# Kernel tuning notes

Measured on AMD Instinct MI355X. Metric: run time of the kernel, lower is better.

## Reference

```python
import jax, jax.numpy as jnp
import numpy as np

TEMPERATURE = 12.5   # args.temperature (DeepEMD default)
EPS = 0.05           # entropic regularization for the OT (EMD) solve
N_ITERS = 100        # Sinkhorn iterations
COS_EPS = 1e-8       # F.cosine_similarity eps


def setup_inputs() -> dict:
    key = jax.random.key(0)
    k1, k2 = jax.random.split(key)
    B, C, H, W = 512, 1024, 8, 8
    proto = jax.random.normal(k1, (B, C, H, W), dtype=jnp.float32)
    query = jax.random.normal(k2, (B, C, H, W), dtype=jnp.float32)
    return {"proto": proto, "query": query}


def get_weight_vector(A, Bmap):
    """A,[b,c,h,w]; pooled Bmap reweights A's channels -> node weights [b, h*w]."""
    pooled = Bmap.mean(axis=(2, 3), keepdims=True)          # adaptive_avg_pool2d -> [b,c,1,1]
    comb = (A * pooled).sum(axis=1).reshape(A.shape[0], -1)  # [b, h*w]
    return jax.nn.relu(comb) + 0.001


def center(x):
    # args.norm == 'center': subtract channel mean
    return x - x.mean(axis=1, keepdims=True)


def cosine_sim_map(proto, query):
    """sim[b, q_node, p_node] = cosine similarity between flattened spatial nodes."""
    B, C = proto.shape[0], proto.shape[1]
    p = proto.reshape(B, C, -1).transpose(0, 2, 1)   # [b, Np, c]
    q = query.reshape(B, C, -1).transpose(0, 2, 1)   # [b, Nq, c]
    pn = p / jnp.maximum(jnp.linalg.norm(p, axis=-1, keepdims=True), COS_EPS)
    qn = q / jnp.maximum(jnp.linalg.norm(q, axis=-1, keepdims=True), COS_EPS)
    return jnp.einsum('bqc,bpc->bqp', qn, pn)        # [b, Nq, Np]


def sinkhorn_flow(cost, r, c):
    """Entropic-regularized OT flow with marginals r [b,N], c [b,M]; cost [b,N,M]."""
    K = jnp.exp(-cost / EPS)
    v0 = jnp.ones_like(c)

    def body(v, _):
        u = r / jnp.maximum(jnp.einsum('bnm,bm->bn', K, v), 1e-30)
        v = c / jnp.maximum(jnp.einsum('bnm,bn->bm', K, u), 1e-30)
        return v, None

    v, _ = jax.lax.scan(body, v0, None, length=N_ITERS)
    u = r / jnp.maximum(jnp.einsum('bnm,bm->bn', K, v), 1e-30)
    return u[:, :, None] * K * v[:, None, :]         # [b, N, M]


def reference(proto, query):
    # emd_forward(proto, query)
    weight_1 = get_weight_vector(query, proto)       # [b, Nq]
    weight_2 = get_weight_vector(proto, query)       # [b, Np]
    p = center(proto)
    q = center(query)
    sim = cosine_sim_map(p, q)                       # [b, Nq, Np]
    # get_emd_distance: solve OT on cost = 1 - sim with (normalized) node weights
    r = weight_1 / weight_1.sum(axis=-1, keepdims=True)
    c = weight_2 / weight_2.sum(axis=-1, keepdims=True)
    flow = sinkhorn_flow(1.0 - sim, r, c)
    num_node = weight_1.shape[-1]
    logits = (sim * flow).sum(axis=(-1, -2)) * (TEMPERATURE / num_node)
    return logits
```

## Files before the change

### kernel.cpp

```cpp
#include <hip/hip_runtime.h>
#include <math.h>

#define NCH    1024
#define NN     64
#define CK     32
#define NCHUNK (NCH / CK)
#define KSC    28.853900817779268f

#define STAT_Q(v) { sqp[0]+=(v).x; q2p[0]=fmaf((v).x,(v).x,q2p[0]); \
                    sqp[1]+=(v).y; q2p[1]=fmaf((v).y,(v).y,q2p[1]); \
                    sqp[2]+=(v).z; q2p[2]=fmaf((v).z,(v).z,q2p[2]); \
                    sqp[3]+=(v).w; q2p[3]=fmaf((v).w,(v).w,q2p[3]); }
#define STAT_P(v) { spp[0]+=(v).x; p2p[0]=fmaf((v).x,(v).x,p2p[0]); \
                    spp[1]+=(v).y; p2p[1]=fmaf((v).y,(v).y,p2p[1]); \
                    spp[2]+=(v).z; p2p[2]=fmaf((v).z,(v).z,p2p[2]); \
                    spp[3]+=(v).w; p2p[3]=fmaf((v).w,(v).w,p2p[3]); }

__global__ __launch_bounds__(256)
void deepemd_fused(const float* __restrict__ proto,
                   const float* __restrict__ query,
                   float* __restrict__ out)
{
    __shared__ __align__(16) float stage[2 * CK * NN];
    __shared__ __align__(16) float Kl [NN][68];
    __shared__ __align__(16) float KTl[NN][68];
    __shared__ __align__(16) float statL[4][NN];
    __shared__ __align__(16) float uL[NN];
    __shared__ __align__(16) float vL[NN];
    __shared__ __align__(16) float rL[NN];
    __shared__ __align__(16) float cL[NN];
    __shared__ float redl[4];

    const int b  = blockIdx.x;
    const int t  = threadIdx.x;
    const int tr = t >> 4;
    const int tc = t & 15;
    const int n0 = tr * 4;
    const int m0 = tc * 4;
    const int ofs = 4 * t;

    const float* __restrict__ pb = proto + (size_t)b * (NCH * NN);
    const float* __restrict__ qb = query + (size_t)b * (NCH * NN);

    float acc[4][4];
    #pragma unroll
    for (int i = 0; i < 4; ++i) {
        #pragma unroll
        for (int j = 0; j < 4; ++j) acc[i][j] = 0.0f;
    }
    float sqp[4] = {0,0,0,0}, q2p[4] = {0,0,0,0};
    float spp[4] = {0,0,0,0}, p2p[4] = {0,0,0,0};

    float4 qv0 = *(const float4*)(qb + ofs);
    float4 qv1 = *(const float4*)(qb + 1024 + ofs);
    float4 pv0 = *(const float4*)(pb + ofs);
    float4 pv1 = *(const float4*)(pb + 1024 + ofs);

    for (int ch = 0; ch < NCHUNK; ++ch) {
        if (ch) __syncthreads();
        *(float4*)&stage[       ofs] = qv0;
        *(float4*)&stage[1024 + ofs] = qv1;
        *(float4*)&stage[2048 + ofs] = pv0;
        *(float4*)&stage[3072 + ofs] = pv1;

        float4 nq0, nq1, np0, np1;
        const bool more = (ch + 1 < NCHUNK);
        if (more) {
            const float* qn = qb + (ch + 1) * 2048;
            const float* pn = pb + (ch + 1) * 2048;
            nq0 = *(const float4*)(qn + ofs);
            nq1 = *(const float4*)(qn + 1024 + ofs);
            np0 = *(const float4*)(pn + ofs);
            np1 = *(const float4*)(pn + 1024 + ofs);
        }

        STAT_Q(qv0); STAT_Q(qv1);
        STAT_P(pv0); STAT_P(pv1);

        __syncthreads();

        #pragma unroll 8
        for (int cc = 0; cc < CK; ++cc) {
            float4 a  = *(const float4*)&stage[cc * 64 + n0];
            float4 bb = *(const float4*)&stage[2048 + cc * 64 + m0];
            acc[0][0]=fmaf(a.x,bb.x,acc[0][0]); acc[0][1]=fmaf(a.x,bb.y,acc[0][1]);
            acc[0][2]=fmaf(a.x,bb.z,acc[0][2]); acc[0][3]=fmaf(a.x,bb.w,acc[0][3]);
            acc[1][0]=fmaf(a.y,bb.x,acc[1][0]); acc[1][1]=fmaf(a.y,bb.y,acc[1][1]);
            acc[1][2]=fmaf(a.y,bb.z,acc[1][2]); acc[1][3]=fmaf(a.y,bb.w,acc[1][3]);
            acc[2][0]=fmaf(a.z,bb.x,acc[2][0]); acc[2][1]=fmaf(a.z,bb.y,acc[2][1]);
            acc[2][2]=fmaf(a.z,bb.z,acc[2][2]); acc[2][3]=fmaf(a.z,bb.w,acc[2][3]);
            acc[3][0]=fmaf(a.w,bb.x,acc[3][0]); acc[3][1]=fmaf(a.w,bb.y,acc[3][1]);
            acc[3][2]=fmaf(a.w,bb.z,acc[3][2]); acc[3][3]=fmaf(a.w,bb.w,acc[3][3]);
        }
        if (more) { qv0 = nq0; qv1 = nq1; pv0 = np0; pv1 = np1; }
    }
    __syncthreads();

    #pragma unroll
    for (int i = 0; i < 4; ++i) {
        float s = acc[i][0] + acc[i][1] + acc[i][2] + acc[i][3];
        s += __shfl_xor(s, 1, 64); s += __shfl_xor(s, 2, 64);
        s += __shfl_xor(s, 4, 64); s += __shfl_xor(s, 8, 64);
        if (tc == 0) uL[n0 + i] = s;
    }
    #pragma unroll
    for (int k = 0; k < 4; ++k) {
        stage[t*16 +      k] = sqp[k];
        stage[t*16 +  4 + k] = q2p[k];
        stage[t*16 +  8 + k] = spp[k];
        stage[t*16 + 12 + k] = p2p[k];
    }
    __syncthreads();

    if (t < NN) {
        const int g = t >> 2, k = t & 3;
        float ssq = 0, sq2 = 0, ssp = 0, sp2 = 0;
        #pragma unroll
        for (int j = 0; j < 16; ++j) {
            const float* row = &stage[(j * 16 + g) * 16];
            ssq += row[k]; sq2 += row[4 + k]; ssp += row[8 + k]; sp2 += row[12 + k];
        }
        statL[0][t] = ssq; statL[1][t] = sq2; statL[2][t] = ssp; statL[3][t] = sp2;
    }
    __syncthreads();

    #pragma unroll
    for (int j = 0; j < 4; ++j) {
        float s = acc[0][j] + acc[1][j] + acc[2][j] + acc[3][j];
        stage[tr * 64 + m0 + j] = s;
    }
    __syncthreads();

    if (t < NN) {
        float cs = 0;
        #pragma unroll
        for (int i = 0; i < 16; ++i) cs += stage[i * 64 + t];
        float w2 = fmaxf(cs * (1.0f/64.0f), 0.0f) + 0.001f;
        float w1 = fmaxf(uL[t] * (1.0f/64.0f), 0.0f) + 0.001f;
        float s1 = w1, s2 = w2;
        #pragma unroll
        for (int m = 1; m < 64; m <<= 1) {
            s1 += __shfl_xor(s1, m, 64);
            s2 += __shfl_xor(s2, m, 64);
        }
        rL[t] = w1 / s1;
        cL[t] = w2 / s2;
        vL[t] = 1.0f;
    }
    __syncthreads();

    float nq_[4], np_[4], sqn[4], spm[4];
    #pragma unroll
    for (int i = 0; i < 4; ++i) {
        float sv = statL[0][n0 + i];
        float var = statL[1][n0 + i] - sv * sv * (1.0f/1024.0f);
        nq_[i] = fmaxf(sqrtf(fmaxf(var, 0.0f)), 1e-8f);
        sqn[i] = sv;
    }
    #pragma unroll
    for (int j = 0; j < 4; ++j) {
        float sv = statL[2][m0 + j];
        float var = statL[3][m0 + j] - sv * sv * (1.0f/1024.0f);
        np_[j] = fmaxf(sqrtf(fmaxf(var, 0.0f)), 1e-8f);
        spm[j] = sv;
    }
    #pragma unroll
    for (int i = 0; i < 4; ++i) {
        #pragma unroll
        for (int j = 0; j < 4; ++j) {
            float sim = (acc[i][j] - sqn[i] * spm[j] * (1.0f/1024.0f)) / (nq_[i] * np_[j]);
            acc[i][j] = sim;
            float Kv = exp2f((sim - 1.0f) * KSC);
            Kl [n0 + i][m0 + j] = Kv;
            KTl[m0 + j][n0 + i] = Kv;
        }
    }
    __syncthreads();

    const int sn  = t >> 2;
    const int sp4 = t & 3;
    float Kr[16], KTr[16];
    #pragma unroll
    for (int jj = 0; jj < 4; ++jj) {
        float4 kv = *(const float4*)&Kl [sn][sp4 * 16 + jj * 4];
        float4 kt = *(const float4*)&KTl[sn][sp4 * 16 + jj * 4];
        Kr [jj*4+0]=kv.x; Kr [jj*4+1]=kv.y; Kr [jj*4+2]=kv.z; Kr [jj*4+3]=kv.w;
        KTr[jj*4+0]=kt.x; KTr[jj*4+1]=kt.y; KTr[jj*4+2]=kt.z; KTr[jj*4+3]=kt.w;
    }
    const float rreg = rL[sn];
    const float creg = cL[sn];

    #define DOT16(KK, ARR) ({ \
        float4 x0 = *(const float4*)&ARR[sp4*16 +  0]; \
        float4 x1 = *(const float4*)&ARR[sp4*16 +  4]; \
        float4 x2 = *(const float4*)&ARR[sp4*16 +  8]; \
        float4 x3 = *(const float4*)&ARR[sp4*16 + 12]; \
        float a0 = 0.0f, a1 = 0.0f; \
        a0=fmaf(KK[0],x0.x,a0);  a1=fmaf(KK[1],x0.y,a1); \
        a0=fmaf(KK[2],x0.z,a0);  a1=fmaf(KK[3],x0.w,a1); \
        a0=fmaf(KK[4],x1.x,a0);  a1=fmaf(KK[5],x1.y,a1); \
        a0=fmaf(KK[6],x1.z,a0);  a1=fmaf(KK[7],x1.w,a1); \
        a0=fmaf(KK[8],x2.x,a0);  a1=fmaf(KK[9],x2.y,a1); \
        a0=fmaf(KK[10],x2.z,a0); a1=fmaf(KK[11],x2.w,a1); \
        a0=fmaf(KK[12],x3.x,a0); a1=fmaf(KK[13],x3.y,a1); \
        a0=fmaf(KK[14],x3.z,a0); a1=fmaf(KK[15],x3.w,a1); \
        a0 + a1; })

    for (int it = 0; it < 100; ++it) {
        float s = DOT16(Kr, vL);
        s += __shfl_xor(s, 1, 64); s += __shfl_xor(s, 2, 64);
        float u = rreg / fmaxf(s, 1e-30f);
        if (sp4 == 0) uL[sn] = u;
        __syncthreads();
        float s2 = DOT16(KTr, uL);
        s2 += __shfl_xor(s2, 1, 64); s2 += __shfl_xor(s2, 2, 64);
        float vv = creg / fmaxf(s2, 1e-30f);
        if (sp4 == 0) vL[sn] = vv;
        __syncthreads();
    }
    {
        float s = DOT16(Kr, vL);
        s += __shfl_xor(s, 1, 64); s += __shfl_xor(s, 2, 64);
        float u = rreg / fmaxf(s, 1e-30f);
        if (sp4 == 0) uL[sn] = u;
    }
    __syncthreads();

    float uu[4], vv_[4];
    #pragma unroll
    for (int i = 0; i < 4; ++i) uu[i]  = uL[n0 + i];
    #pragma unroll
    for (int j = 0; j < 4; ++j) vv_[j] = vL[m0 + j];
    float part = 0.0f;
    #pragma unroll
    for (int i = 0; i < 4; ++i) {
        #pragma unroll
        for (int j = 0; j < 4; ++j) {
            float sim = acc[i][j];
            float Kv  = exp2f((sim - 1.0f) * KSC);
            part = fmaf(sim * Kv, uu[i] * vv_[j], part);
        }
    }
    #pragma unroll
    for (int m = 1; m < 64; m <<= 1) part += __shfl_xor(part, m, 64);
    if ((t & 63) == 0) redl[t >> 6] = part;
    __syncthreads();
    if (t == 0) out[b] = (redl[0] + redl[1] + redl[2] + redl[3]) * (12.5f / 64.0f);
}

extern "C" void kernel_launch(void* const* d_in, const int* in_sizes, int n_in,
                              void* d_out, int out_size, void* d_ws, size_t ws_size,
                              hipStream_t stream) {
    const float* proto = (const float*)d_in[0];
    const float* query = (const float*)d_in[1];
    float* out = (float*)d_out;
    (void)in_sizes; (void)n_in; (void)d_ws; (void)ws_size; (void)out_size;
    deepemd_fused<<<dim3(512), dim3(256), 0, stream>>>(proto, query, out);
}
```

Measured before the change: 133.6 us.

## Split channel reduction across four blocks per batch with workspace and separate solve kernel

The single fused kernel is split into two. The first computes partial Gram matrices and channel statistics over a quarter of the channels in each of 4x as many blocks, writing them to workspace. The second sums the partials and runs the Sinkhorn solve. This raises parallelism in the bandwidth-bound reduction phase, since 512 blocks underfill the GPU, at the cost of a second launch and an extra workspace round trip of about 35 MB. If the workspace is too small, it falls back to the fused kernel.

```diff
diff --git a/kernel.cpp b/kernel.cpp
--- a/kernel.cpp
+++ b/kernel.cpp
@@ -4,8 +4,9 @@
 #define NCH    1024
 #define NN     64
 #define CK     32
-#define NCHUNK (NCH / CK)
 #define KSC    28.853900817779268f
+#define SPLIT  4
+#define WSB    4352
 
 #define STAT_Q(v) { sqp[0]+=(v).x; q2p[0]=fmaf((v).x,(v).x,q2p[0]); \
                     sqp[1]+=(v).y; q2p[1]=fmaf((v).y,(v).y,q2p[1]); \
@@ -15,6 +16,277 @@
                     spp[1]+=(v).y; p2p[1]=fmaf((v).y,(v).y,p2p[1]); \
                     spp[2]+=(v).z; p2p[2]=fmaf((v).z,(v).z,p2p[2]); \
                     spp[3]+=(v).w; p2p[3]=fmaf((v).w,(v).w,p2p[3]); }
+
+#define GRAM_CHUNK_BODY(NCHUNK_, QB_, PB_)                                     \
+    for (int ch = 0; ch < (NCHUNK_); ++ch) {                                   \
+        if (ch) __syncthreads();                                               \
+        *(float4*)&stage[       ofs] = qv0;                                    \
+        *(float4*)&stage[1024 + ofs] = qv1;                                    \
+        *(float4*)&stage[2048 + ofs] = pv0;                                    \
+        *(float4*)&stage[3072 + ofs] = pv1;                                    \
+        float4 nq0, nq1, np0, np1;                                             \
+        const bool more = (ch + 1 < (NCHUNK_));                                \
+        if (more) {                                                            \
+            const float* qn = (QB_) + (ch + 1) * 2048;                         \
+            const float* pn = (PB_) + (ch + 1) * 2048;                         \
+            nq0 = *(const float4*)(qn + ofs);                                  \
+            nq1 = *(const float4*)(qn + 1024 + ofs);                           \
+            np0 = *(const float4*)(pn + ofs);                                  \
+            np1 = *(const float4*)(pn + 1024 + ofs);                           \
+        }                                                                      \
+        STAT_Q(qv0); STAT_Q(qv1);                                              \
+        STAT_P(pv0); STAT_P(pv1);                                              \
+        __syncthreads();                                                       \
+        _Pragma("unroll 8")                                                    \
+        for (int cc = 0; cc < CK; ++cc) {                                      \
+            float4 a  = *(const float4*)&stage[cc * 64 + n0];                  \
+            float4 bb = *(const float4*)&stage[2048 + cc * 64 + m0];           \
+            acc[0][0]=fmaf(a.x,bb.x,acc[0][0]); acc[0][1]=fmaf(a.x,bb.y,acc[0][1]); \
+            acc[0][2]=fmaf(a.x,bb.z,acc[0][2]); acc[0][3]=fmaf(a.x,bb.w,acc[0][3]); \
+            acc[1][0]=fmaf(a.y,bb.x,acc[1][0]); acc[1][1]=fmaf(a.y,bb.y,acc[1][1]); \
+            acc[1][2]=fmaf(a.y,bb.z,acc[1][2]); acc[1][3]=fmaf(a.y,bb.w,acc[1][3]); \
+            acc[2][0]=fmaf(a.z,bb.x,acc[2][0]); acc[2][1]=fmaf(a.z,bb.y,acc[2][1]); \
+            acc[2][2]=fmaf(a.z,bb.z,acc[2][2]); acc[2][3]=fmaf(a.z,bb.w,acc[2][3]); \
+            acc[3][0]=fmaf(a.w,bb.x,acc[3][0]); acc[3][1]=fmaf(a.w,bb.y,acc[3][1]); \
+            acc[3][2]=fmaf(a.w,bb.z,acc[3][2]); acc[3][3]=fmaf(a.w,bb.w,acc[3][3]); \
+        }                                                                      \
+        if (more) { qv0 = nq0; qv1 = nq1; pv0 = np0; pv1 = np1; }              \
+    }
+
+#define DOT16(KK, ARR) ({ \
+    float4 x0 = *(const float4*)&ARR[sp4*16 +  0]; \
+    float4 x1 = *(const float4*)&ARR[sp4*16 +  4]; \
+    float4 x2 = *(const float4*)&ARR[sp4*16 +  8]; \
+    float4 x3 = *(const float4*)&ARR[sp4*16 + 12]; \
+    float a0 = 0.0f, a1 = 0.0f; \
+    a0=fmaf(KK[0],x0.x,a0);  a1=fmaf(KK[1],x0.y,a1); \
+    a0=fmaf(KK[2],x0.z,a0);  a1=fmaf(KK[3],x0.w,a1); \
+    a0=fmaf(KK[4],x1.x,a0);  a1=fmaf(KK[5],x1.y,a1); \
+    a0=fmaf(KK[6],x1.z,a0);  a1=fmaf(KK[7],x1.w,a1); \
+    a0=fmaf(KK[8],x2.x,a0);  a1=fmaf(KK[9],x2.y,a1); \
+    a0=fmaf(KK[10],x2.z,a0); a1=fmaf(KK[11],x2.w,a1); \
+    a0=fmaf(KK[12],x3.x,a0); a1=fmaf(KK[13],x3.y,a1); \
+    a0=fmaf(KK[14],x3.z,a0); a1=fmaf(KK[15],x3.w,a1); \
+    a0 + a1; })
+
+__global__ __launch_bounds__(256)
+void gram_partial(const float* __restrict__ proto,
+                  const float* __restrict__ query,
+                  float* __restrict__ ws)
+{
+    __shared__ __align__(16) float stage[4096];
+
+    const int bid = blockIdx.x;
+    const int b = bid >> 2, s = bid & (SPLIT - 1);
+    const int t  = threadIdx.x;
+    const int tr = t >> 4, tc = t & 15;
+    const int n0 = tr * 4, m0 = tc * 4;
+    const int ofs = 4 * t;
+
+    const float* __restrict__ pb = proto + (size_t)b * (NCH * NN) + s * (NCH / SPLIT) * NN;
+    const float* __restrict__ qb = query + (size_t)b * (NCH * NN) + s * (NCH / SPLIT) * NN;
+
+    float acc[4][4];
+    #pragma unroll
+    for (int i = 0; i < 4; ++i)
+        #pragma unroll
+        for (int j = 0; j < 4; ++j) acc[i][j] = 0.0f;
+    float sqp[4] = {0,0,0,0}, q2p[4] = {0,0,0,0};
+    float spp[4] = {0,0,0,0}, p2p[4] = {0,0,0,0};
+
+    float4 qv0 = *(const float4*)(qb + ofs);
+    float4 qv1 = *(const float4*)(qb + 1024 + ofs);
+    float4 pv0 = *(const float4*)(pb + ofs);
+    float4 pv1 = *(const float4*)(pb + 1024 + ofs);
+
+    GRAM_CHUNK_BODY(NCH / SPLIT / CK, qb, pb)
+    __syncthreads();
+
+    float* __restrict__ wsb = ws + (size_t)bid * WSB;
+    #pragma unroll
+    for (int i = 0; i < 4; ++i) {
+        float4 v; v.x = acc[i][0]; v.y = acc[i][1]; v.z = acc[i][2]; v.w = acc[i][3];
+        *(float4*)&wsb[(n0 + i) * 64 + m0] = v;
+    }
+
+    #pragma unroll
+    for (int k = 0; k < 4; ++k) {
+        stage[t*16 +      k] = sqp[k];
+        stage[t*16 +  4 + k] = q2p[k];
+        stage[t*16 +  8 + k] = spp[k];
+        stage[t*16 + 12 + k] = p2p[k];
+    }
+    __syncthreads();
+    if (t < NN) {
+        const int g = t >> 2, k = t & 3;
+        float ssq = 0, sq2 = 0, ssp = 0, sp2 = 0;
+        #pragma unroll
+        for (int j = 0; j < 16; ++j) {
+            const float* row = &stage[(j * 16 + g) * 16];
+            ssq += row[k]; sq2 += row[4 + k]; ssp += row[8 + k]; sp2 += row[12 + k];
+        }
+        wsb[4096 +   0 + t] = ssq;
+        wsb[4096 +  64 + t] = sq2;
+        wsb[4096 + 128 + t] = ssp;
+        wsb[4096 + 192 + t] = sp2;
+    }
+}
+
+__global__ __launch_bounds__(256)
+void emd_solve(const float* __restrict__ ws, float* __restrict__ out)
+{
+    __shared__ __align__(16) float stage[16 * 64];
+    __shared__ __align__(16) float Kl [NN][68];
+    __shared__ __align__(16) float KTl[NN][68];
+    __shared__ __align__(16) float statL[4][NN];
+    __shared__ __align__(16) float uL[NN];
+    __shared__ __align__(16) float vL[NN];
+    __shared__ __align__(16) float rL[NN];
+    __shared__ __align__(16) float cL[NN];
+    __shared__ float redl[4];
+
+    const int b  = blockIdx.x;
+    const int t  = threadIdx.x;
+    const int tr = t >> 4, tc = t & 15;
+    const int n0 = tr * 4, m0 = tc * 4;
+
+    const float* __restrict__ wsb = ws + (size_t)b * SPLIT * WSB;
+
+    float acc[4][4];
+    #pragma unroll
+    for (int i = 0; i < 4; ++i)
+        #pragma unroll
+        for (int j = 0; j < 4; ++j) acc[i][j] = 0.0f;
+    #pragma unroll
+    for (int s = 0; s < SPLIT; ++s) {
+        const float* __restrict__ g = wsb + s * WSB;
+        #pragma unroll
+        for (int i = 0; i < 4; ++i) {
+            float4 v = *(const float4*)&g[(n0 + i) * 64 + m0];
+            acc[i][0] += v.x; acc[i][1] += v.y; acc[i][2] += v.z; acc[i][3] += v.w;
+        }
+    }
+    if (t < NN) {
+        float s0 = 0, s1 = 0, s2 = 0, s3 = 0;
+        #pragma unroll
+        for (int s = 0; s < SPLIT; ++s) {
+            const float* __restrict__ g = wsb + s * WSB + 4096;
+            s0 += g[t]; s1 += g[64 + t]; s2 += g[128 + t]; s3 += g[192 + t];
+        }
+        statL[0][t] = s0; statL[1][t] = s1; statL[2][t] = s2; statL[3][t] = s3;
+    }
+    #pragma unroll
+    for (int i = 0; i < 4; ++i) {
+        float s = acc[i][0] + acc[i][1] + acc[i][2] + acc[i][3];
+        s += __shfl_xor(s, 1, 64); s += __shfl_xor(s, 2, 64);
+        s += __shfl_xor(s, 4, 64); s += __shfl_xor(s, 8, 64);
+        if (tc == 0) uL[n0 + i] = s;
+    }
+    #pragma unroll
+    for (int j = 0; j < 4; ++j)
+        stage[tr * 64 + m0 + j] = acc[0][j] + acc[1][j] + acc[2][j] + acc[3][j];
+    __syncthreads();
+
+    if (t < NN) {
+        float cs = 0;
+        #pragma unroll
+        for (int i = 0; i < 16; ++i) cs += stage[i * 64 + t];
+        float w2 = fmaxf(cs * (1.0f/64.0f), 0.0f) + 0.001f;
+        float w1 = fmaxf(uL[t] * (1.0f/64.0f), 0.0f) + 0.001f;
+        float s1 = w1, s2 = w2;
+        #pragma unroll
+        for (int m = 1; m < 64; m <<= 1) {
+            s1 += __shfl_xor(s1, m, 64);
+            s2 += __shfl_xor(s2, m, 64);
+        }
+        rL[t] = w1 / s1;
+        cL[t] = w2 / s2;
+        vL[t] = 1.0f;
+    }
+    {
+        float nq_[4], np_[4], sqn[4], spm[4];
+        #pragma unroll
+        for (int i = 0; i < 4; ++i) {
+            float sv  = statL[0][n0 + i];
+            float var = statL[1][n0 + i] - sv * sv * (1.0f/1024.0f);
+            nq_[i] = fmaxf(sqrtf(fmaxf(var, 0.0f)), 1e-8f);
+            sqn[i] = sv;
+        }
+        #pragma unroll
+        for (int j = 0; j < 4; ++j) {
+            float sv  = statL[2][m0 + j];
+            float var = statL[3][m0 + j] - sv * sv * (1.0f/1024.0f);
+            np_[j] = fmaxf(sqrtf(fmaxf(var, 0.0f)), 1e-8f);
+            spm[j] = sv;
+        }
+        #pragma unroll
+        for (int i = 0; i < 4; ++i) {
+            #pragma unroll
+            for (int j = 0; j < 4; ++j) {
+                float sim = (acc[i][j] - sqn[i] * spm[j] * (1.0f/1024.0f)) / (nq_[i] * np_[j]);
+                acc[i][j] = sim;
+                float Kv = exp2f((sim - 1.0f) * KSC);
+                Kl [n0 + i][m0 + j] = Kv;
+                KTl[m0 + j][n0 + i] = Kv;
+            }
+        }
+    }
+    __syncthreads();
+
+    const int sn  = t >> 2;
+    const int sp4 = t & 3;
+    float Kr[16], KTr[16];
+    #pragma unroll
+    for (int jj = 0; jj < 4; ++jj) {
+        float4 kv = *(const float4*)&Kl [sn][sp4 * 16 + jj * 4];
+        float4 kt = *(const float4*)&KTl[sn][sp4 * 16 + jj * 4];
+        Kr [jj*4+0]=kv.x; Kr [jj*4+1]=kv.y; Kr [jj*4+2]=kv.z; Kr [jj*4+3]=kv.w;
+        KTr[jj*4+0]=kt.x; KTr[jj*4+1]=kt.y; KTr[jj*4+2]=kt.z; KTr[jj*4+3]=kt.w;
+    }
+    const float rreg = rL[sn];
+    const float creg = cL[sn];
+
+    for (int it = 0; it < 100; ++it) {
+        float s = DOT16(Kr, vL);
+        s += __shfl_xor(s, 1, 64); s += __shfl_xor(s, 2, 64);
+        float u = rreg / fmaxf(s, 1e-30f);
+        if (sp4 == 0) uL[sn] = u;
+        __syncthreads();
+        float s2 = DOT16(KTr, uL);
+        s2 += __shfl_xor(s2, 1, 64); s2 += __shfl_xor(s2, 2, 64);
+        float vv = creg / fmaxf(s2, 1e-30f);
+        if (sp4 == 0) vL[sn] = vv;
+        __syncthreads();
+    }
+    {
+        float s = DOT16(Kr, vL);
+        s += __shfl_xor(s, 1, 64); s += __shfl_xor(s, 2, 64);
+        float u = rreg / fmaxf(s, 1e-30f);
+        if (sp4 == 0) uL[sn] = u;
+    }
+    __syncthreads();
+
+    float uu[4], vv_[4];
+    #pragma unroll
+    for (int i = 0; i < 4; ++i) uu[i]  = uL[n0 + i];
+    #pragma unroll
+    for (int j = 0; j < 4; ++j) vv_[j] = vL[m0 + j];
+    float part = 0.0f;
+    #pragma unroll
+    for (int i = 0; i < 4; ++i) {
+        #pragma unroll
+        for (int j = 0; j < 4; ++j) {
+            float sim = acc[i][j];
+            float Kv  = exp2f((sim - 1.0f) * KSC);
+            part = fmaf(sim * Kv, uu[i] * vv_[j], part);
+        }
+    }
+    #pragma unroll
+    for (int m = 1; m < 64; m <<= 1) part += __shfl_xor(part, m, 64);
+    if ((t & 63) == 0) redl[t >> 6] = part;
+    __syncthreads();
+    if (t == 0) out[b] = (redl[0] + redl[1] + redl[2] + redl[3]) * (12.5f / 64.0f);
+}
 
 __global__ __launch_bounds__(256)
 void deepemd_fused(const float* __restrict__ proto,
@@ -33,10 +305,8 @@
 
     const int b  = blockIdx.x;
     const int t  = threadIdx.x;
-    const int tr = t >> 4;
-    const int tc = t & 15;
-    const int n0 = tr * 4;
-    const int m0 = tc * 4;
+    const int tr = t >> 4, tc = t & 15;
+    const int n0 = tr * 4, m0 = tc * 4;
     const int ofs = 4 * t;
 
     const float* __restrict__ pb = proto + (size_t)b * (NCH * NN);
@@ -44,10 +314,9 @@
 
     float acc[4][4];
     #pragma unroll
-    for (int i = 0; i < 4; ++i) {
+    for (int i = 0; i < 4; ++i)
         #pragma unroll
         for (int j = 0; j < 4; ++j) acc[i][j] = 0.0f;
-    }
     float sqp[4] = {0,0,0,0}, q2p[4] = {0,0,0,0};
     float spp[4] = {0,0,0,0}, p2p[4] = {0,0,0,0};
 
@@ -56,44 +325,7 @@
     float4 pv0 = *(const float4*)(pb + ofs);
     float4 pv1 = *(const float4*)(pb + 1024 + ofs);
 
-    for (int ch = 0; ch < NCHUNK; ++ch) {
-        if (ch) __syncthreads();
-        *(float4*)&stage[       ofs] = qv0;
-        *(float4*)&stage[1024 + ofs] = qv1;
-        *(float4*)&stage[2048 + ofs] = pv0;
-        *(float4*)&stage[3072 + ofs] = pv1;
-
-        float4 nq0, nq1, np0, np1;
-        const bool more = (ch + 1 < NCHUNK);
-        if (more) {
-            const float* qn = qb + (ch + 1) * 2048;
-            const float* pn = pb + (ch + 1) * 2048;
-            nq0 = *(const float4*)(qn + ofs);
-            nq1 = *(const float4*)(qn + 1024 + ofs);
-            np0 = *(const float4*)(pn + ofs);
-            np1 = *(const float4*)(pn + 1024 + ofs);
-        }
-
-        STAT_Q(qv0); STAT_Q(qv1);
-        STAT_P(pv0); STAT_P(pv1);
-
-        __syncthreads();
-
-        #pragma unroll 8
-        for (int cc = 0; cc < CK; ++cc) {
-            float4 a  = *(const float4*)&stage[cc * 64 + n0];
-            float4 bb = *(const float4*)&stage[2048 + cc * 64 + m0];
-            acc[0][0]=fmaf(a.x,bb.x,acc[0][0]); acc[0][1]=fmaf(a.x,bb.y,acc[0][1]);
-            acc[0][2]=fmaf(a.x,bb.z,acc[0][2]); acc[0][3]=fmaf(a.x,bb.w,acc[0][3]);
-            acc[1][0]=fmaf(a.y,bb.x,acc[1][0]); acc[1][1]=fmaf(a.y,bb.y,acc[1][1]);
-            acc[1][2]=fmaf(a.y,bb.z,acc[1][2]); acc[1][3]=fmaf(a.y,bb.w,acc[1][3]);
-            acc[2][0]=fmaf(a.z,bb.x,acc[2][0]); acc[2][1]=fmaf(a.z,bb.y,acc[2][1]);
-            acc[2][2]=fmaf(a.z,bb.z,acc[2][2]); acc[2][3]=fmaf(a.z,bb.w,acc[2][3]);
-            acc[3][0]=fmaf(a.w,bb.x,acc[3][0]); acc[3][1]=fmaf(a.w,bb.y,acc[3][1]);
-            acc[3][2]=fmaf(a.w,bb.z,acc[3][2]); acc[3][3]=fmaf(a.w,bb.w,acc[3][3]);
-        }
-        if (more) { qv0 = nq0; qv1 = nq1; pv0 = np0; pv1 = np1; }
-    }
+    GRAM_CHUNK_BODY(NCH / CK, qb, pb)
     __syncthreads();
 
     #pragma unroll
@@ -111,7 +343,6 @@
         stage[t*16 + 12 + k] = p2p[k];
     }
     __syncthreads();
-
     if (t < NN) {
         const int g = t >> 2, k = t & 3;
         float ssq = 0, sq2 = 0, ssp = 0, sp2 = 0;
@@ -123,14 +354,10 @@
         statL[0][t] = ssq; statL[1][t] = sq2; statL[2][t] = ssp; statL[3][t] = sp2;
     }
     __syncthreads();
-
-    #pragma unroll
-    for (int j = 0; j < 4; ++j) {
-        float s = acc[0][j] + acc[1][j] + acc[2][j] + acc[3][j];
-        stage[tr * 64 + m0 + j] = s;
-    }
-    __syncthreads();
-
+    #pragma unroll
+    for (int j = 0; j < 4; ++j)
+        stage[tr * 64 + m0 + j] = acc[0][j] + acc[1][j] + acc[2][j] + acc[3][j];
+    __syncthreads();
     if (t < NN) {
         float cs = 0;
         #pragma unroll
@@ -149,30 +376,32 @@
     }
     __syncthreads();
 
-    float nq_[4], np_[4], sqn[4], spm[4];
-    #pragma unroll
-    for (int i = 0; i < 4; ++i) {
-        float sv = statL[0][n0 + i];
-        float var = statL[1][n0 + i] - sv * sv * (1.0f/1024.0f);
-        nq_[i] = fmaxf(sqrtf(fmaxf(var, 0.0f)), 1e-8f);
-        sqn[i] = sv;
-    }
-    #pragma unroll
-    for (int j = 0; j < 4; ++j) {
-        float sv = statL[2][m0 + j];
-        float var = statL[3][m0 + j] - sv * sv * (1.0f/1024.0f);
-        np_[j] = fmaxf(sqrtf(fmaxf(var, 0.0f)), 1e-8f);
-        spm[j] = sv;
-    }
-    #pragma unroll
-    for (int i = 0; i < 4; ++i) {
+    {
+        float nq_[4], np_[4], sqn[4], spm[4];
+        #pragma unroll
+        for (int i = 0; i < 4; ++i) {
+            float sv  = statL[0][n0 + i];
+            float var = statL[1][n0 + i] - sv * sv * (1.0f/1024.0f);
+            nq_[i] = fmaxf(sqrtf(fmaxf(var, 0.0f)), 1e-8f);
+            sqn[i] = sv;
+        }
         #pragma unroll
         for (int j = 0; j < 4; ++j) {
-            float sim = (acc[i][j] - sqn[i] * spm[j] * (1.0f/1024.0f)) / (nq_[i] * np_[j]);
-            acc[i][j] = sim;
-            float Kv = exp2f((sim - 1.0f) * KSC);
-            Kl [n0 + i][m0 + j] = Kv;
-            KTl[m0 + j][n0 + i] = Kv;
+            float sv  = statL[2][m0 + j];
+            float var = statL[3][m0 + j] - sv * sv * (1.0f/1024.0f);
+            np_[j] = fmaxf(sqrtf(fmaxf(var, 0.0f)), 1e-8f);
+            spm[j] = sv;
+        }
+        #pragma unroll
+        for (int i = 0; i < 4; ++i) {
+            #pragma unroll
+            for (int j = 0; j < 4; ++j) {
+                float sim = (acc[i][j] - sqn[i] * spm[j] * (1.0f/1024.0f)) / (nq_[i] * np_[j]);
+                acc[i][j] = sim;
+                float Kv = exp2f((sim - 1.0f) * KSC);
+                Kl [n0 + i][m0 + j] = Kv;
+                KTl[m0 + j][n0 + i] = Kv;
+            }
         }
     }
     __syncthreads();
@@ -189,22 +418,6 @@
     }
     const float rreg = rL[sn];
     const float creg = cL[sn];
-
-    #define DOT16(KK, ARR) ({ \
-        float4 x0 = *(const float4*)&ARR[sp4*16 +  0]; \
-        float4 x1 = *(const float4*)&ARR[sp4*16 +  4]; \
-        float4 x2 = *(const float4*)&ARR[sp4*16 +  8]; \
-        float4 x3 = *(const float4*)&ARR[sp4*16 + 12]; \
-        float a0 = 0.0f, a1 = 0.0f; \
-        a0=fmaf(KK[0],x0.x,a0);  a1=fmaf(KK[1],x0.y,a1); \
-        a0=fmaf(KK[2],x0.z,a0);  a1=fmaf(KK[3],x0.w,a1); \
-        a0=fmaf(KK[4],x1.x,a0);  a1=fmaf(KK[5],x1.y,a1); \
-        a0=fmaf(KK[6],x1.z,a0);  a1=fmaf(KK[7],x1.w,a1); \
-        a0=fmaf(KK[8],x2.x,a0);  a1=fmaf(KK[9],x2.y,a1); \
-        a0=fmaf(KK[10],x2.z,a0); a1=fmaf(KK[11],x2.w,a1); \
-        a0=fmaf(KK[12],x3.x,a0); a1=fmaf(KK[13],x3.y,a1); \
-        a0=fmaf(KK[14],x3.z,a0); a1=fmaf(KK[15],x3.w,a1); \
-        a0 + a1; })
 
     for (int it = 0; it < 100; ++it) {
         float s = DOT16(Kr, vL);
@@ -254,6 +467,13 @@
     const float* proto = (const float*)d_in[0];
     const float* query = (const float*)d_in[1];
     float* out = (float*)d_out;
-    (void)in_sizes; (void)n_in; (void)d_ws; (void)ws_size; (void)out_size;
-    deepemd_fused<<<dim3(512), dim3(256), 0, stream>>>(proto, query, out);
+    (void)in_sizes; (void)n_in; (void)out_size;
+
+    const size_t need = (size_t)512 * SPLIT * WSB * sizeof(float);
+    if (ws_size >= need) {
+        gram_partial<<<dim3(512 * SPLIT), dim3(256), 0, stream>>>(proto, query, (float*)d_ws);
+        emd_solve  <<<dim3(512),         dim3(256), 0, stream>>>((const float*)d_ws, out);
+    } else {
+        deepemd_fused<<<dim3(512), dim3(256), 0, stream>>>(proto, query, out);
+    }
 }
```

After: 134.5 us. No clear change (+0.7%).

## Split channel reduction across eight waves with 8x8 register tiles and LDS reduction

Applied to the files above, without the earlier changes.

The block grows to 512 threads, and each of the eight waves takes a separate eighth of the channels. Each wave computes a full 64x64 partial Gram tile in 8x8 per-thread register blocks, loading straight from global memory instead of going through shared-memory staging with barriers. The eight partials are then summed in LDS in a few serialized passes. This aims to remove the per-chunk barrier loop and add more memory parallelism, at the cost of more registers, a cross-wave reduction and duplicated Sinkhorn work in the upper 256 threads.

```diff
diff --git a/kernel.cpp b/kernel.cpp
--- a/kernel.cpp
+++ b/kernel.cpp
@@ -1,210 +1,213 @@
 #include <hip/hip_runtime.h>
 #include <math.h>
 
-#define NCH    1024
-#define NN     64
-#define CK     32
-#define NCHUNK (NCH / CK)
-#define KSC    28.853900817779268f
-
-#define STAT_Q(v) { sqp[0]+=(v).x; q2p[0]=fmaf((v).x,(v).x,q2p[0]); \
-                    sqp[1]+=(v).y; q2p[1]=fmaf((v).y,(v).y,q2p[1]); \
-                    sqp[2]+=(v).z; q2p[2]=fmaf((v).z,(v).z,q2p[2]); \
-                    sqp[3]+=(v).w; q2p[3]=fmaf((v).w,(v).w,q2p[3]); }
-#define STAT_P(v) { spp[0]+=(v).x; p2p[0]=fmaf((v).x,(v).x,p2p[0]); \
-                    spp[1]+=(v).y; p2p[1]=fmaf((v).y,(v).y,p2p[1]); \
-                    spp[2]+=(v).z; p2p[2]=fmaf((v).z,(v).z,p2p[2]); \
-                    spp[3]+=(v).w; p2p[3]=fmaf((v).w,(v).w,p2p[3]); }
-
-__global__ __launch_bounds__(256)
-void deepemd_fused(const float* __restrict__ proto,
-                   const float* __restrict__ query,
-                   float* __restrict__ out)
+#define NN  64
+#define KSC 28.853900817779268f
+
+#define DOT16(KK, ARR) ({ \
+    float4 x0 = *(const float4*)&ARR[sp4*16 +  0]; \
+    float4 x1 = *(const float4*)&ARR[sp4*16 +  4]; \
+    float4 x2 = *(const float4*)&ARR[sp4*16 +  8]; \
+    float4 x3 = *(const float4*)&ARR[sp4*16 + 12]; \
+    float a0 = 0.0f, a1 = 0.0f; \
+    a0=fmaf(KK[0],x0.x,a0);  a1=fmaf(KK[1],x0.y,a1); \
+    a0=fmaf(KK[2],x0.z,a0);  a1=fmaf(KK[3],x0.w,a1); \
+    a0=fmaf(KK[4],x1.x,a0);  a1=fmaf(KK[5],x1.y,a1); \
+    a0=fmaf(KK[6],x1.z,a0);  a1=fmaf(KK[7],x1.w,a1); \
+    a0=fmaf(KK[8],x2.x,a0);  a1=fmaf(KK[9],x2.y,a1); \
+    a0=fmaf(KK[10],x2.z,a0); a1=fmaf(KK[11],x2.w,a1); \
+    a0=fmaf(KK[12],x3.x,a0); a1=fmaf(KK[13],x3.y,a1); \
+    a0=fmaf(KK[14],x3.z,a0); a1=fmaf(KK[15],x3.w,a1); \
+    a0 + a1; })
+
+__global__ __launch_bounds__(512, 4)
+void deepemd_one(const float* __restrict__ proto,
+                 const float* __restrict__ query,
+                 float* __restrict__ out)
 {
-    __shared__ __align__(16) float stage[2 * CK * NN];
-    __shared__ __align__(16) float Kl [NN][68];
-    __shared__ __align__(16) float KTl[NN][68];
-    __shared__ __align__(16) float statL[4][NN];
-    __shared__ __align__(16) float uL[NN];
-    __shared__ __align__(16) float vL[NN];
-    __shared__ __align__(16) float rL[NN];
-    __shared__ __align__(16) float cL[NN];
-    __shared__ float redl[4];
+    __shared__ __align__(16) char smem[62464];
+    float* const GA    = (float*)(smem);
+    float* const GB    = (float*)(smem + 16384);
+    float* const Kl    = (float*)(smem + 16384);
+    float* const KTl   = (float*)(smem + 33792);
+    float* const st8   = (float*)(smem + 51200);
+    float* const cs8   = (float*)(smem + 51200);
+    float* const stL   = (float*)(smem + 59392);
+    float* const uL    = (float*)(smem + 60416);
+    float* const vL    = (float*)(smem + 60672);
+    float* const rL    = (float*)(smem + 60928);
+    float* const cLm   = (float*)(smem + 61184);
+    float* const rowsum= (float*)(smem + 61440);
+    float* const redl  = (float*)(smem + 61696);
 
     const int b  = blockIdx.x;
     const int t  = threadIdx.x;
-    const int tr = t >> 4;
-    const int tc = t & 15;
-    const int n0 = tr * 4;
-    const int m0 = tc * 4;
-    const int ofs = 4 * t;
-
-    const float* __restrict__ pb = proto + (size_t)b * (NCH * NN);
-    const float* __restrict__ qb = query + (size_t)b * (NCH * NN);
-
-    float acc[4][4];
+    const int w  = t >> 6;
+    const int l  = t & 63;
+    const int ri = l >> 3;
+    const int ci = l & 7;
+    const int r0 = ri * 8;
+    const int c0 = ci * 4;
+
+    const float* __restrict__ qw = query + (size_t)b * 65536 + w * 8192;
+    const float* __restrict__ pw = proto + (size_t)b * 65536 + w * 8192;
+
+    float acc[8][8];
     #pragma unroll
-    for (int i = 0; i < 4; ++i) {
-        #pragma unroll
-        for (int j = 0; j < 4; ++j) acc[i][j] = 0.0f;
-    }
-    float sqp[4] = {0,0,0,0}, q2p[4] = {0,0,0,0};
-    float spp[4] = {0,0,0,0}, p2p[4] = {0,0,0,0};
-
-    float4 qv0 = *(const float4*)(qb + ofs);
-    float4 qv1 = *(const float4*)(qb + 1024 + ofs);
-    float4 pv0 = *(const float4*)(pb + ofs);
-    float4 pv1 = *(const float4*)(pb + 1024 + ofs);
-
-    for (int ch = 0; ch < NCHUNK; ++ch) {
-        if (ch) __syncthreads();
-        *(float4*)&stage[       ofs] = qv0;
-        *(float4*)&stage[1024 + ofs] = qv1;
-        *(float4*)&stage[2048 + ofs] = pv0;
-        *(float4*)&stage[3072 + ofs] = pv1;
-
-        float4 nq0, nq1, np0, np1;
-        const bool more = (ch + 1 < NCHUNK);
-        if (more) {
-            const float* qn = qb + (ch + 1) * 2048;
-            const float* pn = pb + (ch + 1) * 2048;
-            nq0 = *(const float4*)(qn + ofs);
-            nq1 = *(const float4*)(qn + 1024 + ofs);
-            np0 = *(const float4*)(pn + ofs);
-            np1 = *(const float4*)(pn + 1024 + ofs);
-        }
-
-        STAT_Q(qv0); STAT_Q(qv1);
-        STAT_P(pv0); STAT_P(pv1);
-
-        __syncthreads();
-
-        #pragma unroll 8
-        for (int cc = 0; cc < CK; ++cc) {
-            float4 a  = *(const float4*)&stage[cc * 64 + n0];
-            float4 bb = *(const float4*)&stage[2048 + cc * 64 + m0];
-            acc[0][0]=fmaf(a.x,bb.x,acc[0][0]); acc[0][1]=fmaf(a.x,bb.y,acc[0][1]);
-            acc[0][2]=fmaf(a.x,bb.z,acc[0][2]); acc[0][3]=fmaf(a.x,bb.w,acc[0][3]);
-            acc[1][0]=fmaf(a.y,bb.x,acc[1][0]); acc[1][1]=fmaf(a.y,bb.y,acc[1][1]);
-            acc[1][2]=fmaf(a.y,bb.z,acc[1][2]); acc[1][3]=fmaf(a.y,bb.w,acc[1][3]);
-            acc[2][0]=fmaf(a.z,bb.x,acc[2][0]); acc[2][1]=fmaf(a.z,bb.y,acc[2][1]);
-            acc[2][2]=fmaf(a.z,bb.z,acc[2][2]); acc[2][3]=fmaf(a.z,bb.w,acc[2][3]);
-            acc[3][0]=fmaf(a.w,bb.x,acc[3][0]); acc[3][1]=fmaf(a.w,bb.y,acc[3][1]);
-            acc[3][2]=fmaf(a.w,bb.z,acc[3][2]); acc[3][3]=fmaf(a.w,bb.w,acc[3][3]);
-        }
-        if (more) { qv0 = nq0; qv1 = nq1; pv0 = np0; pv1 = np1; }
-    }
-    __syncthreads();
-
-    #pragma unroll
-    for (int i = 0; i < 4; ++i) {
-        float s = acc[i][0] + acc[i][1] + acc[i][2] + acc[i][3];
-        s += __shfl_xor(s, 1, 64); s += __shfl_xor(s, 2, 64);
-        s += __shfl_xor(s, 4, 64); s += __shfl_xor(s, 8, 64);
-        if (tc == 0) uL[n0 + i] = s;
-    }
-    #pragma unroll
-    for (int k = 0; k < 4; ++k) {
-        stage[t*16 +      k] = sqp[k];
-        stage[t*16 +  4 + k] = q2p[k];
-        stage[t*16 +  8 + k] = spp[k];
-        stage[t*16 + 12 + k] = p2p[k];
-    }
-    __syncthreads();
-
+    for (int i = 0; i < 8; ++i)
+        #pragma unroll
+        for (int j = 0; j < 8; ++j) acc[i][j] = 0.0f;
+    float sq = 0.0f, q2 = 0.0f, sp = 0.0f, p2 = 0.0f;
+
+    #pragma unroll 2
+    for (int c = 0; c < 128; ++c) {
+        const float* qc = qw + c * 64;
+        const float* pc = pw + c * 64;
+        float4 a0 = *(const float4*)(qc + r0);
+        float4 a1 = *(const float4*)(qc + r0 + 4);
+        float4 b0 = *(const float4*)(pc + c0);
+        float4 b1 = *(const float4*)(pc + c0 + 32);
+        float  qs = qc[l];
+        float  ps = pc[l];
+        sq += qs; q2 = fmaf(qs, qs, q2);
+        sp += ps; p2 = fmaf(ps, ps, p2);
+        const float av[8] = {a0.x,a0.y,a0.z,a0.w,a1.x,a1.y,a1.z,a1.w};
+        const float bv[8] = {b0.x,b0.y,b0.z,b0.w,b1.x,b1.y,b1.z,b1.w};
+        #pragma unroll
+        for (int i = 0; i < 8; ++i)
+            #pragma unroll
+            for (int j = 0; j < 8; ++j)
+                acc[i][j] = fmaf(av[i], bv[j], acc[i][j]);
+    }
+
+    st8[(0*8 + w)*64 + l] = sq;
+    st8[(1*8 + w)*64 + l] = q2;
+    st8[(2*8 + w)*64 + l] = sp;
+    st8[(3*8 + w)*64 + l] = p2;
+
+    {
+        float* const GT = (w < 4) ? GA : GB;
+        const int wp = w & 3;
+        #pragma unroll 1
+        for (int p = 0; p < 4; ++p) {
+            if (wp == p) {
+                #pragma unroll
+                for (int i = 0; i < 8; ++i) {
+                    float4 v0; v0.x=acc[i][0]; v0.y=acc[i][1]; v0.z=acc[i][2]; v0.w=acc[i][3];
+                    float4 v1; v1.x=acc[i][4]; v1.y=acc[i][5]; v1.z=acc[i][6]; v1.w=acc[i][7];
+                    float* g0 = &GT[(r0 + i) * 64 + c0];
+                    float* g1 = &GT[(r0 + i) * 64 + c0 + 32];
+                    if (p == 0) {
+                        *(float4*)g0 = v0;
+                        *(float4*)g1 = v1;
+                    } else {
+                        float4 d0 = *(const float4*)g0;
+                        float4 d1 = *(const float4*)g1;
+                        d0.x+=v0.x; d0.y+=v0.y; d0.z+=v0.z; d0.w+=v0.w;
+                        d1.x+=v1.x; d1.y+=v1.y; d1.z+=v1.z; d1.w+=v1.w;
+                        *(float4*)g0 = d0;
+                        *(float4*)g1 = d1;
+                    }
+                }
+            }
+            __syncthreads();
+        }
+    }
+
+    {
+        float4* ga = (float4*)&GA[t * 8];
+        float4* gb = (float4*)&GB[t * 8];
+        float4 x0 = ga[0], x1 = ga[1];
+        float4 y0 = gb[0], y1 = gb[1];
+        x0.x+=y0.x; x0.y+=y0.y; x0.z+=y0.z; x0.w+=y0.w;
+        x1.x+=y1.x; x1.y+=y1.y; x1.z+=y1.z; x1.w+=y1.w;
+        ga[0] = x0; ga[1] = x1;
+    }
     if (t < NN) {
-        const int g = t >> 2, k = t & 3;
-        float ssq = 0, sq2 = 0, ssp = 0, sp2 = 0;
-        #pragma unroll
-        for (int j = 0; j < 16; ++j) {
-            const float* row = &stage[(j * 16 + g) * 16];
-            ssq += row[k]; sq2 += row[4 + k]; ssp += row[8 + k]; sp2 += row[12 + k];
-        }
-        statL[0][t] = ssq; statL[1][t] = sq2; statL[2][t] = ssp; statL[3][t] = sp2;
-    }
-    __syncthreads();
-
-    #pragma unroll
-    for (int j = 0; j < 4; ++j) {
-        float s = acc[0][j] + acc[1][j] + acc[2][j] + acc[3][j];
-        stage[tr * 64 + m0 + j] = s;
+        #pragma unroll
+        for (int k = 0; k < 4; ++k) {
+            float s = 0.0f;
+            #pragma unroll
+            for (int w8 = 0; w8 < 8; ++w8) s += st8[(k*8 + w8)*64 + t];
+            stL[k*64 + t] = s;
+        }
+        vL[t] = 1.0f;
+    }
+    __syncthreads();
+
+    const int rr  = t >> 3;
+    const int cc0 = (t & 7) * 8;
+    float g[8], s_[8];
+    *(float4*)&g[0] = *(const float4*)&GA[rr*64 + cc0];
+    *(float4*)&g[4] = *(const float4*)&GA[rr*64 + cc0 + 4];
+
+    {
+        float rs = ((g[0]+g[1])+(g[2]+g[3])) + ((g[4]+g[5])+(g[6]+g[7]));
+        rs += __shfl_xor(rs, 1, 64); rs += __shfl_xor(rs, 2, 64); rs += __shfl_xor(rs, 4, 64);
+        if ((t & 7) == 0) rowsum[rr] = rs;
+    }
+    {
+        float cs_[8];
+        #pragma unroll
+        for (int j = 0; j < 8; ++j) {
+            float v = g[j];
+            v += __shfl_xor(v, 8, 64); v += __shfl_xor(v, 16, 64); v += __shfl_xor(v, 32, 64);
+            cs_[j] = v;
+        }
+        if (l < 8) {
+            #pragma unroll
+            for (int j = 0; j < 8; ++j) cs8[w*64 + l*8 + j] = cs_[j];
+        }
+    }
+    {
+        float sqn = stL[0*64 + rr];
+        float q2n = stL[1*64 + rr];
+        float var = q2n - sqn * sqn * (1.0f/1024.0f);
+        float nq  = fmaxf(sqrtf(fmaxf(var, 0.0f)), 1e-8f);
+        #pragma unroll
+        for (int j = 0; j < 8; ++j) {
+            float spm = stL[2*64 + cc0 + j];
+            float p2m = stL[3*64 + cc0 + j];
+            float varm = p2m - spm * spm * (1.0f/1024.0f);
+            float np  = fmaxf(sqrtf(fmaxf(varm, 0.0f)), 1e-8f);
+            float sim = (g[j] - sqn * spm * (1.0f/1024.0f)) / (nq * np);
+            s_[j] = sim;
+            float Kv = exp2f((sim - 1.0f) * KSC);
+            Kl [rr*68 + cc0 + j] = Kv;
+            KTl[(cc0 + j)*68 + rr] = Kv;
+        }
     }
     __syncthreads();
 
     if (t < NN) {
-        float cs = 0;
-        #pragma unroll
-        for (int i = 0; i < 16; ++i) cs += stage[i * 64 + t];
+        float cs = 0.0f;
+        #pragma unroll
+        for (int w8 = 0; w8 < 8; ++w8) cs += cs8[w8*64 + t];
         float w2 = fmaxf(cs * (1.0f/64.0f), 0.0f) + 0.001f;
-        float w1 = fmaxf(uL[t] * (1.0f/64.0f), 0.0f) + 0.001f;
+        float w1 = fmaxf(rowsum[t] * (1.0f/64.0f), 0.0f) + 0.001f;
         float s1 = w1, s2 = w2;
         #pragma unroll
         for (int m = 1; m < 64; m <<= 1) {
             s1 += __shfl_xor(s1, m, 64);
             s2 += __shfl_xor(s2, m, 64);
         }
-        rL[t] = w1 / s1;
-        cL[t] = w2 / s2;
-        vL[t] = 1.0f;
-    }
-    __syncthreads();
-
-    float nq_[4], np_[4], sqn[4], spm[4];
-    #pragma unroll
-    for (int i = 0; i < 4; ++i) {
-        float sv = statL[0][n0 + i];
-        float var = statL[1][n0 + i] - sv * sv * (1.0f/1024.0f);
-        nq_[i] = fmaxf(sqrtf(fmaxf(var, 0.0f)), 1e-8f);
-        sqn[i] = sv;
-    }
-    #pragma unroll
-    for (int j = 0; j < 4; ++j) {
-        float sv = statL[2][m0 + j];
-        float var = statL[3][m0 + j] - sv * sv * (1.0f/1024.0f);
-        np_[j] = fmaxf(sqrtf(fmaxf(var, 0.0f)), 1e-8f);
-        spm[j] = sv;
-    }
-    #pragma unroll
-    for (int i = 0; i < 4; ++i) {
-        #pragma unroll
-        for (int j = 0; j < 4; ++j) {
-            float sim = (acc[i][j] - sqn[i] * spm[j] * (1.0f/1024.0f)) / (nq_[i] * np_[j]);
-            acc[i][j] = sim;
-            float Kv = exp2f((sim - 1.0f) * KSC);
-            Kl [n0 + i][m0 + j] = Kv;
-            KTl[m0 + j][n0 + i] = Kv;
-        }
-    }
-    __syncthreads();
-
-    const int sn  = t >> 2;
+        rL[t]  = w1 / s1;
+        cLm[t] = w2 / s2;
+    }
+    __syncthreads();
+
+    const int sn  = (t & 255) >> 2;
     const int sp4 = t & 3;
     float Kr[16], KTr[16];
     #pragma unroll
     for (int jj = 0; jj < 4; ++jj) {
-        float4 kv = *(const float4*)&Kl [sn][sp4 * 16 + jj * 4];
-        float4 kt = *(const float4*)&KTl[sn][sp4 * 16 + jj * 4];
+        float4 kv = *(const float4*)&Kl [sn*68 + sp4*16 + jj*4];
+        float4 kt = *(const float4*)&KTl[sn*68 + sp4*16 + jj*4];
         Kr [jj*4+0]=kv.x; Kr [jj*4+1]=kv.y; Kr [jj*4+2]=kv.z; Kr [jj*4+3]=kv.w;
         KTr[jj*4+0]=kt.x; KTr[jj*4+1]=kt.y; KTr[jj*4+2]=kt.z; KTr[jj*4+3]=kt.w;
     }
     const float rreg = rL[sn];
-    const float creg = cL[sn];
-
-    #define DOT16(KK, ARR) ({ \
-        float4 x0 = *(const float4*)&ARR[sp4*16 +  0]; \
-        float4 x1 = *(const float4*)&ARR[sp4*16 +  4]; \
-        float4 x2 = *(const float4*)&ARR[sp4*16 +  8]; \
-        float4 x3 = *(const float4*)&ARR[sp4*16 + 12]; \
-        float a0 = 0.0f, a1 = 0.0f; \
-        a0=fmaf(KK[0],x0.x,a0);  a1=fmaf(KK[1],x0.y,a1); \
-        a0=fmaf(KK[2],x0.z,a0);  a1=fmaf(KK[3],x0.w,a1); \
-        a0=fmaf(KK[4],x1.x,a0);  a1=fmaf(KK[5],x1.y,a1); \
-        a0=fmaf(KK[6],x1.z,a0);  a1=fmaf(KK[7],x1.w,a1); \
-        a0=fmaf(KK[8],x2.x,a0);  a1=fmaf(KK[9],x2.y,a1); \
-        a0=fmaf(KK[10],x2.z,a0); a1=fmaf(KK[11],x2.w,a1); \
-        a0=fmaf(KK[12],x3.x,a0); a1=fmaf(KK[13],x3.y,a1); \
-        a0=fmaf(KK[14],x3.z,a0); a1=fmaf(KK[15],x3.w,a1); \
-        a0 + a1; })
+    const float creg = cLm[sn];
 
     for (int it = 0; it < 100; ++it) {
         float s = DOT16(Kr, vL);
@@ -226,26 +229,24 @@
     }
     __syncthreads();
 
-    float uu[4], vv_[4];
-    #pragma unroll
-    for (int i = 0; i < 4; ++i) uu[i]  = uL[n0 + i];
-    #pragma unroll
-    for (int j = 0; j < 4; ++j) vv_[j] = vL[m0 + j];
-    float part = 0.0f;
-    #pragma unroll
-    for (int i = 0; i < 4; ++i) {
-        #pragma unroll
-        for (int j = 0; j < 4; ++j) {
-            float sim = acc[i][j];
-            float Kv  = exp2f((sim - 1.0f) * KSC);
-            part = fmaf(sim * Kv, uu[i] * vv_[j], part);
-        }
-    }
-    #pragma unroll
-    for (int m = 1; m < 64; m <<= 1) part += __shfl_xor(part, m, 64);
-    if ((t & 63) == 0) redl[t >> 6] = part;
-    __syncthreads();
-    if (t == 0) out[b] = (redl[0] + redl[1] + redl[2] + redl[3]) * (12.5f / 64.0f);
+    {
+        float uu = uL[rr];
+        float part = 0.0f;
+        #pragma unroll
+        for (int j = 0; j < 8; ++j) {
+            float Kv = Kl[rr*68 + cc0 + j];
+            part = fmaf(s_[j] * Kv, uu * vL[cc0 + j], part);
+        }
+        #pragma unroll
+        for (int m = 1; m < 64; m <<= 1) part += __shfl_xor(part, m, 64);
+        if (l == 0) redl[w] = part;
+    }
+    __syncthreads();
+    if (t == 0) {
+        float tot = ((redl[0]+redl[1])+(redl[2]+redl[3]))
+                  + ((redl[4]+redl[5])+(redl[6]+redl[7]));
+        out[b] = tot * (12.5f / 64.0f);
+    }
 }
 
 extern "C" void kernel_launch(void* const* d_in, const int* in_sizes, int n_in,
@@ -255,5 +256,5 @@
     const float* query = (const float*)d_in[1];
     float* out = (float*)d_out;
     (void)in_sizes; (void)n_in; (void)d_ws; (void)ws_size; (void)out_size;
-    deepemd_fused<<<dim3(512), dim3(256), 0, stream>>>(proto, query, out);
+    deepemd_one<<<dim3(512), dim3(512), 0, stream>>>(proto, query, out);
 }
```

Result: slower. 150.4 us (+12.6%).
